# Kernel tuning notes

Measured on AMD Instinct MI355X. Metric: run time of the kernel, lower is better.

Reference implementation:

```python
import jax, jax.numpy as jnp
import numpy as np

N_PATHS = 1_000_000
N_LINKS = 50_000
K_HOPS = 8


def setup_inputs() -> dict:
    key = jax.random.key(0)
    k1, k2, k3 = jax.random.split(key, 3)
    # path features; column 1 is the injected traffic A (as in X[:, path_og.stop-2])
    P = jax.random.uniform(k1, (N_PATHS, 3), dtype=jnp.float32)
    # raw link capacity feature data.L; forward divides by 1000 -> capacity in [100, 300]
    L = jax.random.uniform(k2, (N_LINKS, 1), dtype=jnp.float32) * 2.0e5 + 1.0e5
    # k-th hop of each path: which path (global node id == local id since paths come first)
    pl_paths = jnp.broadcast_to(jnp.arange(N_PATHS, dtype=jnp.int32), (K_HOPS, N_PATHS))
    # which link node id is traversed at hop k (global ids: links occupy [N_PATHS, N_PATHS+N_LINKS))
    pl_edges = jax.random.randint(k3, (K_HOPS, N_PATHS), N_PATHS, N_PATHS + N_LINKS, dtype=jnp.int32)
    return {"P": P, "L": L, "pl_paths": pl_paths, "pl_edges": pl_edges,
            "n_paths": N_PATHS, "n_links": N_LINKS, "num_iterations": 3}


def reference(P, L, pl_paths, pl_edges, n_paths, n_links, num_iterations):
    B = 32  # buffer size
    A = P[:, 1]                      # per-path injected traffic [n_paths]
    cap = L[:, 0] / 1000.0           # link capacity (X[is_l, link_og.start]) [n_links]
    e_local = pl_edges - n_paths     # link-local indices [K, n_paths]

    def update_traffic(bp_links):
        # Original: at step k, decay traffic by prev step's blocking then scatter.
        # Equivalent reorder: scatter this step, then decay with this step's links
        # (decayed traffic is only consumed at step k+1).
        def step(carry, xs):
            traffic, T = carry
            pk, ek = xs
            T = T + jax.ops.segment_sum(traffic[pk], ek, num_segments=n_links)
            traffic = traffic.at[pk].multiply(1.0 - bp_links[ek])
            return (traffic, T), None
        T0 = jnp.zeros((n_links,), dtype=A.dtype)
        (_, T), _ = jax.lax.scan(step, (A, T0), (pl_paths, e_local))
        return T

    bp = 0.5 * jnp.ones((n_links,), dtype=A.dtype)
    rho = jnp.zeros((n_links,), dtype=A.dtype)
    for _ in range(num_iterations):
        T = update_traffic(bp)
        rho = T / cap
        bp = (1.0 - rho) * rho ** B / (1.0 - rho ** (B + 1) + 1e-8)

    # Erlang-like mean-queue series: res = pi0 * (1 + sum_{m=1}^{32} m*rho^m) / 32
    pi0 = (1.0 - rho) / (1.0 - rho ** (B + 1))
    m = jnp.arange(B + 1, dtype=A.dtype)            # [33]
    coeff = jnp.where(m == 0, 1.0, m)
    Lq = pi0 * jnp.sum(coeff * rho[:, None] ** m, axis=1) / 32.0   # [n_links]
    pi0_final = pi0 * rho ** B                       # pi_0 after the 32-step loop

    # final per-path delay aggregation over all path-link edges
    X_l = Lq * 32000.0 / L[:, 0]                     # [n_links]
    E = X_l[e_local.reshape(-1)]                     # [K*n_paths]
    res = jax.ops.segment_sum(E, pl_paths.reshape(-1), num_segments=n_paths)
    return res, jnp.stack([Lq, rho, pi0_final], axis=1)
```

## Files before the change

kernel.cpp:

```cpp
#include <hip/hip_runtime.h>

#define KHOPS  8
#define BS     1024
#define MAXL   50176
#define HCHUNK 25088
#define HWORDS (HCHUNK / 2)
#define P1     8
#define MAXGRID 256
#define MINGRID 64
#define TSCALE  2048.0f
#define XSCALE  131072.0f

typedef unsigned short u16;
typedef unsigned int   u32;

__global__ void convert_kernel(const int* __restrict__ pl_edges,
                               const float* __restrict__ P,
                               u16*   __restrict__ e16,
                               float* __restrict__ A,
                               u16*   __restrict__ bpq,
                               int n_edges, int n_paths, int n_links) {
    int i = blockIdx.x * blockDim.x + threadIdx.x;
    if (i < n_edges) e16[i] = (u16)(pl_edges[i] - n_paths);
    if (i < n_paths) A[i] = P[3 * i + 1];
    if (i < n_links) bpq[i] = 32768;
}

__global__ __launch_bounds__(BS) void scatter_kernel(
        const float* __restrict__ A,
        const u16*   __restrict__ e16,
        const u16*   __restrict__ bpq,
        u32*         __restrict__ Trep,
        int n_paths, int n_links, int nwords) {
    __shared__ u16 bpl[MAXL];
    __shared__ u32 h[HWORDS];
    const int tid = threadIdx.x;
    const int nthreads = gridDim.x * BS;

    for (int i = tid; i < n_links; i += BS) bpl[i] = bpq[i];

    u32* Tmine = Trep + (size_t)blockIdx.x * nwords;
    const int nchunks = (n_links + HCHUNK - 1) / HCHUNK;

    for (int c = 0; c < nchunks; ++c) {
        const int base = c * HCHUNK;

        for (int i = tid; i < HWORDS; i += BS) h[i] = 0u;
        __syncthreads();

        for (int p = (blockIdx.x * BS + tid) * 2; p < n_paths; p += 2 * nthreads) {
            u32 ep[KHOPS];
#pragma unroll
            for (int k = 0; k < KHOPS; ++k)
                ep[k] = *(const u32*)&e16[k * n_paths + p];

            float2 a = *(const float2*)&A[p];
            float t0 = a.x, t1 = a.y;
#pragma unroll
            for (int k = 0; k < KHOPS; ++k) {
                u32 l0 = ep[k] & 0xffffu;
                u32 l1 = ep[k] >> 16;
                float at0 = (float)(65536 - (int)bpl[l0]) * (1.0f / 65536.0f);
                float at1 = (float)(65536 - (int)bpl[l1]) * (1.0f / 65536.0f);
                u32 c0 = l0 - base, c1 = l1 - base;
                if (c0 < HCHUNK)
                    atomicAdd(&h[c0 >> 1],
                              __float2uint_rn(t0 * TSCALE) << ((c0 & 1) << 4));
                if (c1 < HCHUNK)
                    atomicAdd(&h[c1 >> 1],
                              __float2uint_rn(t1 * TSCALE) << ((c1 & 1) << 4));
                t0 *= at0;
                t1 *= at1;
            }
        }
        __syncthreads();

        const int wbase = base >> 1;
        for (int i = tid; i < HWORDS; i += BS) {
            int gw = wbase + i;
            if (gw < nwords) Tmine[gw] = h[i];
        }
        __syncthreads();
    }
}

__global__ void merge_kernel(const u32* __restrict__ Trep,
                             u32* __restrict__ partial,
                             int n_links, int nwords, int G) {
    int w = blockIdx.x * blockDim.x + threadIdx.x;
    int q = blockIdx.y;
    if (w >= nwords) return;
    u32 slo = 0, shi = 0;
    for (int r = q; r < G; r += P1) {
        u32 v = Trep[(size_t)r * nwords + w];
        slo += v & 0xffffu;
        shi += v >> 16;
    }
    *(uint2*)&partial[(size_t)q * n_links + 2 * w] = make_uint2(slo, shi);
}

__global__ void link_update_kernel(const float* __restrict__ L,
                                   const u32*   __restrict__ partial,
                                   u16*         __restrict__ bpq,
                                   float*       __restrict__ rho_out,
                                   int n_links) {
    int l = blockIdx.x * blockDim.x + threadIdx.x;
    if (l >= n_links) return;
    u32 s = 0;
#pragma unroll
    for (int q = 0; q < P1; ++q)
        s += partial[(size_t)q * n_links + l];
    float T = (float)s * (1.0f / TSCALE);
    float cap = L[l] * (1.0f / 1000.0f);
    float rho = T / cap;
    rho_out[l] = rho;
    float r2 = rho * rho, r4 = r2 * r2, r8 = r4 * r4, r16 = r8 * r8;
    float r32 = r16 * r16;
    float r33 = r32 * rho;
    float bp = (1.0f - rho) * r32 / (1.0f - r33 + 1e-8f);
    u32 bfix = __float2uint_rn(bp * 65536.0f);
    bpq[l] = (u16)(bfix > 65535u ? 65535u : bfix);
}

__global__ void epilogue_kernel(const float* __restrict__ L,
                                const float* __restrict__ rho_in,
                                u16*         __restrict__ xq,
                                float*       __restrict__ out_links,
                                int n_links) {
    int l = blockIdx.x * blockDim.x + threadIdx.x;
    if (l >= n_links) return;
    float rho = rho_in[l];
    float r2 = rho * rho, r4 = r2 * r2, r8 = r4 * r4, r16 = r8 * r8;
    float r32 = r16 * r16;
    float r33 = r32 * rho;
    float pi0 = (1.0f - rho) / (1.0f - r33);

    float S = 1.0f, rp = 1.0f;
#pragma unroll
    for (int m = 1; m <= 32; ++m) { rp *= rho; S += (float)m * rp; }

    float Lq   = pi0 * S * (1.0f / 32.0f);
    float pi0f = pi0 * r32;
    float X    = Lq * 32000.0f / L[l];

    u32 xfix = __float2uint_rn(X * XSCALE);
    xq[l] = (u16)(xfix > 65535u ? 65535u : xfix);
    out_links[3 * l + 0] = Lq;
    out_links[3 * l + 1] = rho;
    out_links[3 * l + 2] = pi0f;
}

__global__ __launch_bounds__(BS) void gather_kernel(
        const u16* __restrict__ e16,
        const u16* __restrict__ xq,
        float*     __restrict__ res,
        int n_paths, int n_links) {
    __shared__ u16 xl[MAXL];
    const int tid = threadIdx.x;
    for (int i = tid; i < n_links; i += BS) xl[i] = xq[i];
    __syncthreads();

    const int nthreads = gridDim.x * BS;
    for (int p = (blockIdx.x * BS + tid) * 2; p < n_paths; p += 2 * nthreads) {
        u32 s0 = 0, s1 = 0;
#pragma unroll
        for (int k = 0; k < KHOPS; ++k) {
            u32 ep = *(const u32*)&e16[k * n_paths + p];
            s0 += xl[ep & 0xffffu];
            s1 += xl[ep >> 16];
        }
        *(float2*)&res[p] = make_float2((float)s0 * (1.0f / XSCALE),
                                        (float)s1 * (1.0f / XSCALE));
    }
}

extern "C" void kernel_launch(void* const* d_in, const int* in_sizes, int n_in,
                              void* d_out, int out_size, void* d_ws, size_t ws_size,
                              hipStream_t stream) {
    const float* P        = (const float*)d_in[0];
    const float* L        = (const float*)d_in[1];
    const int*   pl_edges = (const int*)d_in[3];

    const int n_paths = in_sizes[0] / 3;
    const int n_links = in_sizes[1];
    const int n_edges = KHOPS * n_paths;
    const int nwords  = (n_links + 1) / 2;
    const int num_iterations = 3;

    char* w = (char*)d_ws;
    u16*   e16 = (u16*)w;                     w += (size_t)n_edges * 2;
    w = (char*)(((size_t)w + 15) & ~15ull);
    float* A   = (float*)w;                   w += (size_t)n_paths * 4;
    float* rho = (float*)w;                   w += (size_t)n_links * 4;
    u16*   bpq = (u16*)w;                     w += (size_t)n_links * 2;
    u16*   xq  = (u16*)w;                     w += (size_t)n_links * 2;
    w = (char*)(((size_t)w + 15) & ~15ull);
    u32* partial = (u32*)w;                   w += (size_t)P1 * n_links * 4;
    u32* Trep    = (u32*)w;

    size_t bytes_left = ws_size - (size_t)((char*)Trep - (char*)d_ws);
    int G = (int)(bytes_left / ((size_t)nwords * 4));
    if (G > MAXGRID) G = MAXGRID;
    G &= ~7;
    if (G < MINGRID) G = MINGRID;

    float* res       = (float*)d_out;
    float* out_links = res + n_paths;

    const int bs = 256;
    const int gl = (n_links + bs - 1) / bs;
    const int gc = (n_edges + bs - 1) / bs;
    const int gw2 = (nwords + bs - 1) / bs;

    convert_kernel<<<gc, bs, 0, stream>>>(pl_edges, P, e16, A, bpq,
                                          n_edges, n_paths, n_links);
    for (int it = 0; it < num_iterations; ++it) {
        scatter_kernel<<<G, BS, 0, stream>>>(A, e16, bpq, Trep,
                                             n_paths, n_links, nwords);
        merge_kernel<<<dim3(gw2, P1), bs, 0, stream>>>(Trep, partial,
                                                       n_links, nwords, G);
        link_update_kernel<<<gl, bs, 0, stream>>>(L, partial, bpq, rho, n_links);
    }
    epilogue_kernel<<<gl, bs, 0, stream>>>(L, rho, xq, out_links, n_links);
    gather_kernel<<<MAXGRID, BS, 0, stream>>>(e16, xq, res, n_paths, n_links);
}
```

Baseline: 209.9 us.

## Quantize blocking table to u8 so full link histogram fits in LDS

Shrinks the per-link blocking-probability table to 8-bit so the shared table and a full-width packed histogram fit together in LDS. This removes the two-pass chunked scatter and the redundant edge reads and work it caused. Adds a specialized first-iteration scatter using the constant initial blocking probability, and widens scatter and gather to four paths per thread with vector loads. Coarser quantization of blocking probability may reduce accuracy, and the large LDS footprint limits occupancy.

```diff
diff --git a/kernel.cpp b/kernel.cpp
--- a/kernel.cpp
+++ b/kernel.cpp
@@ -3,14 +3,13 @@
 #define KHOPS  8
 #define BS     1024
 #define MAXL   50176
-#define HCHUNK 25088
-#define HWORDS (HCHUNK / 2)
+#define HWORDS (MAXL / 2)
 #define P1     8
-#define MAXGRID 256
-#define MINGRID 64
+#define GRID   256
 #define TSCALE  2048.0f
 #define XSCALE  131072.0f
 
+typedef unsigned char  u8;
 typedef unsigned short u16;
 typedef unsigned int   u32;
 
@@ -18,70 +17,90 @@
                                const float* __restrict__ P,
                                u16*   __restrict__ e16,
                                float* __restrict__ A,
-                               u16*   __restrict__ bpq,
-                               int n_edges, int n_paths, int n_links) {
+                               int n_edges, int n_paths) {
     int i = blockIdx.x * blockDim.x + threadIdx.x;
     if (i < n_edges) e16[i] = (u16)(pl_edges[i] - n_paths);
     if (i < n_paths) A[i] = P[3 * i + 1];
-    if (i < n_links) bpq[i] = 32768;
-}
-
-__global__ __launch_bounds__(BS) void scatter_kernel(
+}
+
+__device__ __forceinline__ void deposit(u32* h, u32 link, float t) {
+    atomicAdd(&h[link >> 1], __float2uint_rn(t * TSCALE) << ((link & 1) << 4));
+}
+
+__global__ __launch_bounds__(BS) void scatter_first(
         const float* __restrict__ A,
         const u16*   __restrict__ e16,
-        const u16*   __restrict__ bpq,
         u32*         __restrict__ Trep,
-        int n_paths, int n_links, int nwords) {
-    __shared__ u16 bpl[MAXL];
+        int n_paths, int nwords) {
     __shared__ u32 h[HWORDS];
     const int tid = threadIdx.x;
     const int nthreads = gridDim.x * BS;
 
+    for (int i = tid; i < HWORDS; i += BS) h[i] = 0u;
+    __syncthreads();
+
+    for (int p = (blockIdx.x * BS + tid) * 4; p < n_paths; p += 4 * nthreads) {
+        uint2 ep[KHOPS];
+#pragma unroll
+        for (int k = 0; k < KHOPS; ++k)
+            ep[k] = *(const uint2*)&e16[k * n_paths + p];
+        float4 a = *(const float4*)&A[p];
+        float t0 = a.x, t1 = a.y, t2 = a.z, t3 = a.w;
+#pragma unroll
+        for (int k = 0; k < KHOPS; ++k) {
+            deposit(h, ep[k].x & 0xffffu, t0);
+            deposit(h, ep[k].x >> 16,     t1);
+            deposit(h, ep[k].y & 0xffffu, t2);
+            deposit(h, ep[k].y >> 16,     t3);
+            t0 *= 0.5f; t1 *= 0.5f; t2 *= 0.5f; t3 *= 0.5f;
+        }
+    }
+    __syncthreads();
+
+    u32* Tmine = Trep + (size_t)blockIdx.x * nwords;
+    for (int i = tid; i < nwords; i += BS) Tmine[i] = h[i];
+}
+
+__global__ __launch_bounds__(BS) void scatter_rest(
+        const float* __restrict__ A,
+        const u16*   __restrict__ e16,
+        const u8*    __restrict__ bpq,
+        u32*         __restrict__ Trep,
+        int n_paths, int n_links, int nwords) {
+    __shared__ u8  bpl[MAXL];
+    __shared__ u32 h[HWORDS];
+    const int tid = threadIdx.x;
+    const int nthreads = gridDim.x * BS;
+
     for (int i = tid; i < n_links; i += BS) bpl[i] = bpq[i];
+    for (int i = tid; i < HWORDS; i += BS) h[i] = 0u;
+    __syncthreads();
+
+    for (int p = (blockIdx.x * BS + tid) * 4; p < n_paths; p += 4 * nthreads) {
+        uint2 ep[KHOPS];
+#pragma unroll
+        for (int k = 0; k < KHOPS; ++k)
+            ep[k] = *(const uint2*)&e16[k * n_paths + p];
+        float4 a = *(const float4*)&A[p];
+        float t0 = a.x, t1 = a.y, t2 = a.z, t3 = a.w;
+#pragma unroll
+        for (int k = 0; k < KHOPS; ++k) {
+            u32 l0 = ep[k].x & 0xffffu, l1 = ep[k].x >> 16;
+            u32 l2 = ep[k].y & 0xffffu, l3 = ep[k].y >> 16;
+            deposit(h, l0, t0);
+            deposit(h, l1, t1);
+            deposit(h, l2, t2);
+            deposit(h, l3, t3);
+            t0 *= (float)(256 - (int)bpl[l0]) * (1.0f / 256.0f);
+            t1 *= (float)(256 - (int)bpl[l1]) * (1.0f / 256.0f);
+            t2 *= (float)(256 - (int)bpl[l2]) * (1.0f / 256.0f);
+            t3 *= (float)(256 - (int)bpl[l3]) * (1.0f / 256.0f);
+        }
+    }
+    __syncthreads();
 
     u32* Tmine = Trep + (size_t)blockIdx.x * nwords;
-    const int nchunks = (n_links + HCHUNK - 1) / HCHUNK;
-
-    for (int c = 0; c < nchunks; ++c) {
-        const int base = c * HCHUNK;
-
-        for (int i = tid; i < HWORDS; i += BS) h[i] = 0u;
-        __syncthreads();
-
-        for (int p = (blockIdx.x * BS + tid) * 2; p < n_paths; p += 2 * nthreads) {
-            u32 ep[KHOPS];
-#pragma unroll
-            for (int k = 0; k < KHOPS; ++k)
-                ep[k] = *(const u32*)&e16[k * n_paths + p];
-
-            float2 a = *(const float2*)&A[p];
-            float t0 = a.x, t1 = a.y;
-#pragma unroll
-            for (int k = 0; k < KHOPS; ++k) {
-                u32 l0 = ep[k] & 0xffffu;
-                u32 l1 = ep[k] >> 16;
-                float at0 = (float)(65536 - (int)bpl[l0]) * (1.0f / 65536.0f);
-                float at1 = (float)(65536 - (int)bpl[l1]) * (1.0f / 65536.0f);
-                u32 c0 = l0 - base, c1 = l1 - base;
-                if (c0 < HCHUNK)
-                    atomicAdd(&h[c0 >> 1],
-                              __float2uint_rn(t0 * TSCALE) << ((c0 & 1) << 4));
-                if (c1 < HCHUNK)
-                    atomicAdd(&h[c1 >> 1],
-                              __float2uint_rn(t1 * TSCALE) << ((c1 & 1) << 4));
-                t0 *= at0;
-                t1 *= at1;
-            }
-        }
-        __syncthreads();
-
-        const int wbase = base >> 1;
-        for (int i = tid; i < HWORDS; i += BS) {
-            int gw = wbase + i;
-            if (gw < nwords) Tmine[gw] = h[i];
-        }
-        __syncthreads();
-    }
+    for (int i = tid; i < nwords; i += BS) Tmine[i] = h[i];
 }
 
 __global__ void merge_kernel(const u32* __restrict__ Trep,
@@ -101,7 +120,7 @@
 
 __global__ void link_update_kernel(const float* __restrict__ L,
                                    const u32*   __restrict__ partial,
-                                   u16*         __restrict__ bpq,
+                                   u8*          __restrict__ bpq,
                                    float*       __restrict__ rho_out,
                                    int n_links) {
     int l = blockIdx.x * blockDim.x + threadIdx.x;
@@ -118,8 +137,8 @@
     float r32 = r16 * r16;
     float r33 = r32 * rho;
     float bp = (1.0f - rho) * r32 / (1.0f - r33 + 1e-8f);
-    u32 bfix = __float2uint_rn(bp * 65536.0f);
-    bpq[l] = (u16)(bfix > 65535u ? 65535u : bfix);
+    u32 bfix = __float2uint_rn(bp * 256.0f);
+    bpq[l] = (u8)(bfix > 255u ? 255u : bfix);
 }
 
 __global__ void epilogue_kernel(const float* __restrict__ L,
@@ -161,16 +180,20 @@
     __syncthreads();
 
     const int nthreads = gridDim.x * BS;
-    for (int p = (blockIdx.x * BS + tid) * 2; p < n_paths; p += 2 * nthreads) {
-        u32 s0 = 0, s1 = 0;
+    for (int p = (blockIdx.x * BS + tid) * 4; p < n_paths; p += 4 * nthreads) {
+        u32 s0 = 0, s1 = 0, s2 = 0, s3 = 0;
 #pragma unroll
         for (int k = 0; k < KHOPS; ++k) {
-            u32 ep = *(const u32*)&e16[k * n_paths + p];
-            s0 += xl[ep & 0xffffu];
-            s1 += xl[ep >> 16];
+            uint2 ep = *(const uint2*)&e16[k * n_paths + p];
+            s0 += xl[ep.x & 0xffffu];
+            s1 += xl[ep.x >> 16];
+            s2 += xl[ep.y & 0xffffu];
+            s3 += xl[ep.y >> 16];
         }
-        *(float2*)&res[p] = make_float2((float)s0 * (1.0f / XSCALE),
-                                        (float)s1 * (1.0f / XSCALE));
+        *(float4*)&res[p] = make_float4((float)s0 * (1.0f / XSCALE),
+                                        (float)s1 * (1.0f / XSCALE),
+                                        (float)s2 * (1.0f / XSCALE),
+                                        (float)s3 * (1.0f / XSCALE));
     }
 }
 
@@ -185,24 +208,20 @@
     const int n_links = in_sizes[1];
     const int n_edges = KHOPS * n_paths;
     const int nwords  = (n_links + 1) / 2;
-    const int num_iterations = 3;
 
     char* w = (char*)d_ws;
     u16*   e16 = (u16*)w;                     w += (size_t)n_edges * 2;
     w = (char*)(((size_t)w + 15) & ~15ull);
     float* A   = (float*)w;                   w += (size_t)n_paths * 4;
     float* rho = (float*)w;                   w += (size_t)n_links * 4;
-    u16*   bpq = (u16*)w;                     w += (size_t)n_links * 2;
+    u8*    bpq = (u8*)w;                      w += (size_t)n_links;
+    w = (char*)(((size_t)w + 15) & ~15ull);
     u16*   xq  = (u16*)w;                     w += (size_t)n_links * 2;
     w = (char*)(((size_t)w + 15) & ~15ull);
     u32* partial = (u32*)w;                   w += (size_t)P1 * n_links * 4;
     u32* Trep    = (u32*)w;
 
-    size_t bytes_left = ws_size - (size_t)((char*)Trep - (char*)d_ws);
-    int G = (int)(bytes_left / ((size_t)nwords * 4));
-    if (G > MAXGRID) G = MAXGRID;
-    G &= ~7;
-    if (G < MINGRID) G = MINGRID;
+    const int G = GRID;
 
     float* res       = (float*)d_out;
     float* out_links = res + n_paths;
@@ -212,15 +231,18 @@
     const int gc = (n_edges + bs - 1) / bs;
     const int gw2 = (nwords + bs - 1) / bs;
 
-    convert_kernel<<<gc, bs, 0, stream>>>(pl_edges, P, e16, A, bpq,
-                                          n_edges, n_paths, n_links);
-    for (int it = 0; it < num_iterations; ++it) {
-        scatter_kernel<<<G, BS, 0, stream>>>(A, e16, bpq, Trep,
-                                             n_paths, n_links, nwords);
+    convert_kernel<<<gc, bs, 0, stream>>>(pl_edges, P, e16, A, n_edges, n_paths);
+
+    for (int it = 0; it < 3; ++it) {
+        if (it == 0)
+            scatter_first<<<G, BS, 0, stream>>>(A, e16, Trep, n_paths, nwords);
+        else
+            scatter_rest<<<G, BS, 0, stream>>>(A, e16, bpq, Trep,
+                                               n_paths, n_links, nwords);
         merge_kernel<<<dim3(gw2, P1), bs, 0, stream>>>(Trep, partial,
                                                        n_links, nwords, G);
         link_update_kernel<<<gl, bs, 0, stream>>>(L, partial, bpq, rho, n_links);
     }
     epilogue_kernel<<<gl, bs, 0, stream>>>(L, rho, xq, out_links, n_links);
-    gather_kernel<<<MAXGRID, BS, 0, stream>>>(e16, xq, res, n_paths, n_links);
-}
+    gather_kernel<<<GRID, BS, 0, stream>>>(e16, xq, res, n_paths, n_links);
+}
```

After: 191.8 us. 8.6% less time.
